# Optimization experiments

Hardware: AMD Instinct MI355X
Metric: run time of the kernel (lower is better)

Reference implementation:

```python
import jax, jax.numpy as jnp
import numpy as np

N = 100000      # nodes
E = 3200000     # edges (avg degree 32)
F_IN = 128      # input features
HID = 16        # hidden channels (hardcoded in Net)
C = 8           # num_classes


def setup_inputs() -> dict:
    key = jax.random.key(0)
    ks = jax.random.split(key, 6)
    x = jax.random.normal(ks[0], (N, F_IN), dtype=jnp.float32)
    edge_index = jax.random.randint(ks[1], (2, E), 0, N, dtype=jnp.int32)
    W1 = jax.random.normal(ks[2], (F_IN, HID), dtype=jnp.float32) / np.sqrt(F_IN)
    b1 = jnp.zeros((HID,), dtype=jnp.float32)
    W2 = jax.random.normal(ks[3], (HID, C), dtype=jnp.float32) / np.sqrt(HID)
    b2 = jnp.zeros((C,), dtype=jnp.float32)
    return {"x": x, "edge_index": edge_index, "W1": W1, "b1": b1, "W2": W2, "b2": b2}


def _gcn_conv(h, W, b, src, dst, norm):
    # GCNConv: x' = D^{-1/2} (A + I) D^{-1/2} (x W) + b
    h = h @ W                                  # [N, out] transform first (small out dim)
    msg = h[src] * norm[:, None]               # gather + edge normalization  [E+N, out]
    agg = jax.ops.segment_sum(msg, dst, num_segments=N)  # scatter-add to targets
    return agg + b


def reference(x, edge_index, W1, b1, W2, b2):
    row, col = edge_index[0], edge_index[1]
    loop = jnp.arange(N, dtype=row.dtype)
    src = jnp.concatenate([row, loop])         # add self-loops
    dst = jnp.concatenate([col, loop])
    # symmetric normalization: deg over aggregation targets (incl. self-loops)
    deg = jax.ops.segment_sum(jnp.ones_like(dst, dtype=jnp.float32), dst, num_segments=N)
    dinv = jnp.where(deg > 0, jax.lax.rsqrt(deg), 0.0)
    norm = dinv[src] * dinv[dst]               # [E+N]

    h = jax.nn.relu(_gcn_conv(x, W1, b1, src, dst, norm))
    # F.dropout with training=False is the identity (inference reference)
    out = _gcn_conv(h, W2, b2, src, dst, norm)
    return jax.nn.log_softmax(out, axis=1)
```

## Files before the change

kernel.cpp:

```cpp
#include <hip/hip_runtime.h>

#define NN 100000
#define EE 3200000
#define FIN 128
#define HID 16
#define NC 8

#define CHUNK 12500
#define NBLK 256
#define BW 256
#define NBUK ((NN + BW - 1) / BW)
#define EPT 13
#define BSTG 10240
#define BEPT 10

__device__ __forceinline__ unsigned bf16pair(float a, float b) {
    unsigned ua = __float_as_uint(a), ub = __float_as_uint(b);
    ua = ua + 0x7fffu + ((ua >> 16) & 1u);
    ub = ub + 0x7fffu + ((ub >> 16) & 1u);
    return (ua >> 16) | (ub & 0xffff0000u);
}

__global__ __launch_bounds__(1024) void k_hist(const int* __restrict__ col,
                                               unsigned* __restrict__ hist_g) {
    __shared__ unsigned h[NBUK];
    int t = threadIdx.x;
    for (int i = t; i < NBUK; i += 1024) h[i] = 0u;
    __syncthreads();
    int base = blockIdx.x * CHUNK;
    for (int i = t; i < CHUNK; i += 1024) {
        int d = col[base + i];
        atomicAdd(&h[d >> 8], 1u);
    }
    __syncthreads();
    for (int b = t; b < NBUK; b += 1024)
        hist_g[(size_t)b * NBLK + blockIdx.x] = h[b];
}

__global__ __launch_bounds__(256) void k_scan_blocks(const unsigned* __restrict__ hist_g,
                                                     unsigned* __restrict__ blockbase,
                                                     unsigned* __restrict__ totals) {
    __shared__ unsigned sc[NBLK];
    int b = blockIdx.x, t = threadIdx.x;
    unsigned v = hist_g[(size_t)b * NBLK + t];
    sc[t] = v;
    __syncthreads();
    for (int off = 1; off < NBLK; off <<= 1) {
        unsigned x = (t >= off) ? sc[t - off] : 0u;
        __syncthreads();
        sc[t] += x;
        __syncthreads();
    }
    blockbase[(size_t)b * NBLK + t] = sc[t] - v;
    if (t == NBLK - 1) totals[b] = sc[t];
}

__global__ __launch_bounds__(512) void k_scan_buckets(const unsigned* __restrict__ totals,
                                                      unsigned* __restrict__ bucket_base) {
    __shared__ unsigned sc[512];
    int t = threadIdx.x;
    unsigned v = (t < NBUK) ? totals[t] : 0u;
    sc[t] = v;
    __syncthreads();
    for (int off = 1; off < 512; off <<= 1) {
        unsigned x = (t >= off) ? sc[t - off] : 0u;
        __syncthreads();
        sc[t] += x;
        __syncthreads();
    }
    if (t < NBUK) bucket_base[t] = sc[t] - v;
    if (t == NBUK - 1) bucket_base[NBUK] = sc[t];
}

__global__ __launch_bounds__(1024) void k_binscatter(const int* __restrict__ row,
                                                     const int* __restrict__ col,
                                                     const unsigned* __restrict__ blockbase,
                                                     const unsigned* __restrict__ bucket_base,
                                                     unsigned* __restrict__ bins_pk) {
    __shared__ unsigned s_cnt[NBUK];
    __shared__ unsigned s_start[NBUK];
    __shared__ unsigned s_off[NBUK];
    __shared__ unsigned s_bb[NBUK];
    __shared__ unsigned stg[CHUNK];
    __shared__ unsigned short bktid[CHUNK];
    int t = threadIdx.x;
    for (int i = t; i < NBUK; i += 1024) {
        s_cnt[i] = 0u;
        s_bb[i] = bucket_base[i] + blockbase[(size_t)i * NBLK + blockIdx.x];
    }
    __syncthreads();
    int base = blockIdx.x * CHUNK;
    unsigned val[EPT];
    unsigned short bk[EPT];
    #pragma unroll
    for (int k = 0; k < EPT; ++k) {
        int i = t + k * 1024;
        if (i < CHUNK) {
            int s = row[base + i];
            int d = col[base + i];
            unsigned b = (unsigned)d >> 8;
            val[k] = (unsigned)s | ((unsigned)(d & 255) << 17);
            bk[k] = (unsigned short)b;
            atomicAdd(&s_cnt[b], 1u);
        }
    }
    __syncthreads();
    for (int off = 1; off < NBUK; off <<= 1) {
        unsigned v = 0u;
        if (t < NBUK && t >= off) v = s_cnt[t - off];
        __syncthreads();
        if (t < NBUK) s_cnt[t] += v;
        __syncthreads();
    }
    if (t < NBUK) {
        unsigned st = (t == 0) ? 0u : s_cnt[t - 1];
        s_start[t] = st;
        s_off[t] = st;
    }
    __syncthreads();
    #pragma unroll
    for (int k = 0; k < EPT; ++k) {
        int i = t + k * 1024;
        if (i < CHUNK) {
            unsigned b = bk[k];
            unsigned r = atomicAdd(&s_off[b], 1u);
            stg[r] = val[k];
            bktid[r] = (unsigned short)b;
        }
    }
    __syncthreads();
    for (int i = t; i < CHUNK; i += 1024) {
        unsigned b = bktid[i];
        bins_pk[s_bb[b] + ((unsigned)i - s_start[b])] = stg[i];
    }
}

__global__ __launch_bounds__(1024) void k_build(const unsigned* __restrict__ bins_pk,
                                                const unsigned* __restrict__ bucket_base,
                                                unsigned* __restrict__ row_ptr,
                                                float* __restrict__ dinv,
                                                unsigned* __restrict__ srcsort) {
    __shared__ unsigned cnt[BW];
    __shared__ unsigned startn[BW];
    __shared__ unsigned offn[BW];
    __shared__ unsigned stg[BSTG];
    int t = threadIdx.x, b = blockIdx.x;
    if (t < BW) cnt[t] = 0u;
    __syncthreads();
    unsigned start = bucket_base[b], end = bucket_base[b + 1];
    unsigned m = end - start;
    unsigned val[BEPT];
    unsigned char dl[BEPT];
    #pragma unroll
    for (int k = 0; k < BEPT; ++k) {
        unsigned i = t + k * 1024u;
        if (i < m) {
            unsigned w = bins_pk[start + i];
            val[k] = w & 0x1FFFFu;
            dl[k] = (unsigned char)(w >> 17);
            atomicAdd(&cnt[dl[k]], 1u);
        }
    }
    __syncthreads();
    for (int off = 1; off < BW; off <<= 1) {
        unsigned v = 0u;
        if (t < BW && t >= off) v = cnt[t - off];
        __syncthreads();
        if (t < BW) cnt[t] += v;
        __syncthreads();
    }
    if (t < BW) {
        unsigned st = (t == 0) ? 0u : cnt[t - 1];
        startn[t] = st;
        offn[t] = st;
        int node = b * BW + t;
        if (node < NN) {
            row_ptr[node] = start + st;
            dinv[node] = rsqrtf(1.0f + (float)(cnt[t] - st));
        }
    }
    if (b == 0 && t == 0) row_ptr[NN] = EE;
    __syncthreads();
    #pragma unroll
    for (int k = 0; k < BEPT; ++k) {
        unsigned i = t + k * 1024u;
        if (i < m) {
            unsigned r = atomicAdd(&offn[dl[k]], 1u);
            stg[r] = val[k];
        }
    }
    __syncthreads();
    for (unsigned i = t; i < m; i += 1024u)
        srcsort[start + i] = stg[i];
}

__global__ __launch_bounds__(256) void k_gemm1(const float* __restrict__ x,
                                               const float* __restrict__ W1,
                                               const float* __restrict__ dinv,
                                               unsigned* __restrict__ hs1b) {
    __shared__ float w1s[FIN * HID];
    __shared__ float xs[64 * 132];
    int t = threadIdx.x;
    int r0 = blockIdx.x * 64;
    for (int i = t; i < FIN * HID; i += 256) w1s[i] = W1[i];
    int maxr = NN - r0; if (maxr > 64) maxr = 64;
    const float4* x4 = reinterpret_cast<const float4*>(x + (size_t)r0 * FIN);
    #pragma unroll
    for (int i = 0; i < 8; ++i) {
        int fi = t + i * 256;
        int f = fi * 4;
        int r = f >> 7, k = f & 127;
        if (r < maxr) {
            float4 v = x4[fi];
            *reinterpret_cast<float4*>(&xs[r * 132 + k]) = v;
        }
    }
    __syncthreads();
    int r = t >> 2;
    int cg = (t & 3) * 4;
    if (r < maxr) {
        float4 acc = {0.f, 0.f, 0.f, 0.f};
        const float* xr = &xs[r * 132];
        #pragma unroll 4
        for (int k = 0; k < FIN; ++k) {
            float xv = xr[k];
            const float4 w = *reinterpret_cast<const float4*>(&w1s[k * HID + cg]);
            acc.x += xv * w.x; acc.y += xv * w.y; acc.z += xv * w.z; acc.w += xv * w.w;
        }
        int rr = r0 + r;
        float di = dinv[rr];
        uint2 pk;
        pk.x = bf16pair(acc.x * di, acc.y * di);
        pk.y = bf16pair(acc.z * di, acc.w * di);
        *reinterpret_cast<uint2*>(&hs1b[(rr << 3) + (cg >> 1)]) = pk;
    }
}

__global__ __launch_bounds__(256) void k_l1(const unsigned* __restrict__ row_ptr,
                                            const unsigned* __restrict__ srcsort,
                                            const unsigned* __restrict__ hs1b,
                                            const float* __restrict__ dinv,
                                            const float* __restrict__ W2,
                                            const float* __restrict__ b1,
                                            unsigned* __restrict__ hs2b) {
    __shared__ float htile[32 * 17];
    __shared__ float w2s[HID * NC];
    int t = threadIdx.x;
    if (t < HID * NC) w2s[t] = W2[t];
    int g = t >> 3;
    int c2 = t & 7;
    int n = blockIdx.x * 32 + g;
    unsigned e0 = row_ptr[n], e1 = row_ptr[n + 1];
    float a0 = 0.f, a1 = 0.f;
    unsigned e = e0;
    for (; e + 3 < e1; e += 4) {
        int s0 = srcsort[e];
        int s1 = srcsort[e + 1];
        int s2 = srcsort[e + 2];
        int s3 = srcsort[e + 3];
        unsigned v0 = hs1b[(s0 << 3) + c2];
        unsigned v1 = hs1b[(s1 << 3) + c2];
        unsigned v2 = hs1b[(s2 << 3) + c2];
        unsigned v3 = hs1b[(s3 << 3) + c2];
        a0 += __uint_as_float(v0 << 16) + __uint_as_float(v1 << 16)
            + __uint_as_float(v2 << 16) + __uint_as_float(v3 << 16);
        a1 += __uint_as_float(v0 & 0xffff0000u) + __uint_as_float(v1 & 0xffff0000u)
            + __uint_as_float(v2 & 0xffff0000u) + __uint_as_float(v3 & 0xffff0000u);
    }
    for (; e < e1; ++e) {
        unsigned v = hs1b[((int)srcsort[e] << 3) + c2];
        a0 += __uint_as_float(v << 16);
        a1 += __uint_as_float(v & 0xffff0000u);
    }
    {
        unsigned v = hs1b[(n << 3) + c2];
        a0 += __uint_as_float(v << 16);
        a1 += __uint_as_float(v & 0xffff0000u);
    }
    float di = dinv[n];
    int c = c2 * 2;
    htile[g * 17 + c]     = fmaxf(a0 * di + b1[c], 0.f);
    htile[g * 17 + c + 1] = fmaxf(a1 * di + b1[c + 1], 0.f);
    __syncthreads();
    if (t < 128) {
        int n2 = t >> 2, j2 = t & 3;
        const float* hr = &htile[n2 * 17];
        float oa = 0.f, ob = 0.f;
        #pragma unroll
        for (int k = 0; k < HID; ++k) {
            float hv = hr[k];
            oa += hv * w2s[k * NC + 2 * j2];
            ob += hv * w2s[k * NC + 2 * j2 + 1];
        }
        int node2 = blockIdx.x * 32 + n2;
        float d2 = dinv[node2];
        hs2b[(node2 << 2) + j2] = bf16pair(oa * d2, ob * d2);
    }
}

__global__ __launch_bounds__(256) void k_l2(const unsigned* __restrict__ row_ptr,
                                            const unsigned* __restrict__ srcsort,
                                            const unsigned* __restrict__ hs2b,
                                            const float* __restrict__ dinv,
                                            const float* __restrict__ b2,
                                            float* __restrict__ out) {
    int t = threadIdx.x;
    int g = t >> 2;
    int c2 = t & 3;
    int n = blockIdx.x * 64 + g;
    if (n >= NN) return;
    unsigned e0 = row_ptr[n], e1 = row_ptr[n + 1];
    float a0 = 0.f, a1 = 0.f;
    unsigned e = e0;
    for (; e + 3 < e1; e += 4) {
        int s0 = srcsort[e];
        int s1 = srcsort[e + 1];
        int s2 = srcsort[e + 2];
        int s3 = srcsort[e + 3];
        unsigned v0 = hs2b[(s0 << 2) + c2];
        unsigned v1 = hs2b[(s1 << 2) + c2];
        unsigned v2 = hs2b[(s2 << 2) + c2];
        unsigned v3 = hs2b[(s3 << 2) + c2];
        a0 += __uint_as_float(v0 << 16) + __uint_as_float(v1 << 16)
            + __uint_as_float(v2 << 16) + __uint_as_float(v3 << 16);
        a1 += __uint_as_float(v0 & 0xffff0000u) + __uint_as_float(v1 & 0xffff0000u)
            + __uint_as_float(v2 & 0xffff0000u) + __uint_as_float(v3 & 0xffff0000u);
    }
    for (; e < e1; ++e) {
        unsigned v = hs2b[((int)srcsort[e] << 2) + c2];
        a0 += __uint_as_float(v << 16);
        a1 += __uint_as_float(v & 0xffff0000u);
    }
    {
        unsigned v = hs2b[(n << 2) + c2];
        a0 += __uint_as_float(v << 16);
        a1 += __uint_as_float(v & 0xffff0000u);
    }
    float di = dinv[n];
    int c = c2 * 2;
    float v0 = a0 * di + b2[c];
    float v1 = a1 * di + b2[c + 1];
    float m = fmaxf(v0, v1);
    m = fmaxf(m, __shfl_xor(m, 1, 4));
    m = fmaxf(m, __shfl_xor(m, 2, 4));
    float s = expf(v0 - m) + expf(v1 - m);
    s += __shfl_xor(s, 1, 4);
    s += __shfl_xor(s, 2, 4);
    float ls = logf(s);
    float2 o = {v0 - m - ls, v1 - m - ls};
    *reinterpret_cast<float2*>(&out[(n << 3) + c]) = o;
}

extern "C" void kernel_launch(void* const* d_in, const int* in_sizes, int n_in,
                              void* d_out, int out_size, void* d_ws, size_t ws_size,
                              hipStream_t stream) {
    const float* x   = (const float*)d_in[0];
    const int*   ei  = (const int*)d_in[1];
    const float* W1  = (const float*)d_in[2];
    const float* b1  = (const float*)d_in[3];
    const float* W2  = (const float*)d_in[4];
    const float* b2  = (const float*)d_in[5];
    float* out = (float*)d_out;

    const int* row = ei;
    const int* col = ei + EE;

    float*    ws          = (float*)d_ws;
    float*    dinv        = ws;
    unsigned* hs1b        = (unsigned*)(dinv + NN);
    unsigned* hs2b        = hs1b + (size_t)NN * 8;
    unsigned* row_ptr     = hs2b + (size_t)NN * 4;
    unsigned* hist_g      = row_ptr + NN + 1;
    unsigned* blockbase   = hist_g + (size_t)NBUK * NBLK;
    unsigned* totals      = blockbase + (size_t)NBUK * NBLK;
    unsigned* bucket_base = totals + NBUK;
    unsigned* bins_pk     = bucket_base + NBUK + 1;
    unsigned* srcsort     = bins_pk + EE;

    k_hist        <<<NBLK, 1024, 0, stream>>>(col, hist_g);
    k_scan_blocks <<<NBUK, NBLK, 0, stream>>>(hist_g, blockbase, totals);
    k_scan_buckets<<<1, 512, 0, stream>>>(totals, bucket_base);
    k_binscatter  <<<NBLK, 1024, 0, stream>>>(row, col, blockbase, bucket_base, bins_pk);
    k_build       <<<NBUK, 1024, 0, stream>>>(bins_pk, bucket_base, row_ptr, dinv, srcsort);
    k_gemm1       <<<(NN + 63) / 64, 256, 0, stream>>>(x, W1, dinv, hs1b);
    k_l1          <<<NN / 32, 256, 0, stream>>>(row_ptr, srcsort, hs1b, dinv, W2, b1, hs2b);
    k_l2          <<<(NN + 63) / 64, 256, 0, stream>>>(row_ptr, srcsort, hs2b, dinv, b2, out);
}
```

Baseline: 114.9 us.

## Replace histogram+scan bucketing with fixed-capacity buckets and atomic cursors

Drops the global histogram kernel and the two prefix-scan kernels. Each binscatter block now reserves its slice of a bucket by doing an atomicAdd on a per-bucket global cursor, and writes into fixed-capacity bucket regions of CAP entries. The CSR offsets become (start,end) pairs per node, because bucket regions are no longer contiguous. This removes two extra launches and a full pass over col. The cost is a bucket-overflow risk if any bucket gets more than 9216 edges (the mean is about 8192), plus padded, non-deterministic edge ordering within buckets.

```diff
diff --git a/kernel.cpp b/kernel.cpp
--- a/kernel.cpp
+++ b/kernel.cpp
@@ -11,8 +11,8 @@
 #define BW 256
 #define NBUK ((NN + BW - 1) / BW)
 #define EPT 13
-#define BSTG 10240
-#define BEPT 10
+#define CAP 9216
+#define BEPT 9
 
 __device__ __forceinline__ unsigned bf16pair(float a, float b) {
     unsigned ua = __float_as_uint(a), ub = __float_as_uint(b);
@@ -21,73 +21,23 @@
     return (ua >> 16) | (ub & 0xffff0000u);
 }
 
-__global__ __launch_bounds__(1024) void k_hist(const int* __restrict__ col,
-                                               unsigned* __restrict__ hist_g) {
-    __shared__ unsigned h[NBUK];
-    int t = threadIdx.x;
-    for (int i = t; i < NBUK; i += 1024) h[i] = 0u;
-    __syncthreads();
-    int base = blockIdx.x * CHUNK;
-    for (int i = t; i < CHUNK; i += 1024) {
-        int d = col[base + i];
-        atomicAdd(&h[d >> 8], 1u);
-    }
-    __syncthreads();
-    for (int b = t; b < NBUK; b += 1024)
-        hist_g[(size_t)b * NBLK + blockIdx.x] = h[b];
-}
-
-__global__ __launch_bounds__(256) void k_scan_blocks(const unsigned* __restrict__ hist_g,
-                                                     unsigned* __restrict__ blockbase,
-                                                     unsigned* __restrict__ totals) {
-    __shared__ unsigned sc[NBLK];
-    int b = blockIdx.x, t = threadIdx.x;
-    unsigned v = hist_g[(size_t)b * NBLK + t];
-    sc[t] = v;
-    __syncthreads();
-    for (int off = 1; off < NBLK; off <<= 1) {
-        unsigned x = (t >= off) ? sc[t - off] : 0u;
-        __syncthreads();
-        sc[t] += x;
-        __syncthreads();
-    }
-    blockbase[(size_t)b * NBLK + t] = sc[t] - v;
-    if (t == NBLK - 1) totals[b] = sc[t];
-}
-
-__global__ __launch_bounds__(512) void k_scan_buckets(const unsigned* __restrict__ totals,
-                                                      unsigned* __restrict__ bucket_base) {
-    __shared__ unsigned sc[512];
-    int t = threadIdx.x;
-    unsigned v = (t < NBUK) ? totals[t] : 0u;
-    sc[t] = v;
-    __syncthreads();
-    for (int off = 1; off < 512; off <<= 1) {
-        unsigned x = (t >= off) ? sc[t - off] : 0u;
-        __syncthreads();
-        sc[t] += x;
-        __syncthreads();
-    }
-    if (t < NBUK) bucket_base[t] = sc[t] - v;
-    if (t == NBUK - 1) bucket_base[NBUK] = sc[t];
+__global__ __launch_bounds__(512) void k_zero_cursor(unsigned* __restrict__ cursor) {
+    int t = threadIdx.x;
+    if (t < NBUK) cursor[t] = 0u;
 }
 
 __global__ __launch_bounds__(1024) void k_binscatter(const int* __restrict__ row,
                                                      const int* __restrict__ col,
-                                                     const unsigned* __restrict__ blockbase,
-                                                     const unsigned* __restrict__ bucket_base,
+                                                     unsigned* __restrict__ cursor,
                                                      unsigned* __restrict__ bins_pk) {
     __shared__ unsigned s_cnt[NBUK];
     __shared__ unsigned s_start[NBUK];
     __shared__ unsigned s_off[NBUK];
-    __shared__ unsigned s_bb[NBUK];
+    __shared__ unsigned s_gb[NBUK];
     __shared__ unsigned stg[CHUNK];
     __shared__ unsigned short bktid[CHUNK];
     int t = threadIdx.x;
-    for (int i = t; i < NBUK; i += 1024) {
-        s_cnt[i] = 0u;
-        s_bb[i] = bucket_base[i] + blockbase[(size_t)i * NBLK + blockIdx.x];
-    }
+    for (int i = t; i < NBUK; i += 1024) s_cnt[i] = 0u;
     __syncthreads();
     int base = blockIdx.x * CHUNK;
     unsigned val[EPT];
@@ -105,6 +55,9 @@
         }
     }
     __syncthreads();
+    for (int i = t; i < NBUK; i += 1024)
+        s_gb[i] = atomicAdd(&cursor[i], s_cnt[i]);
+    __syncthreads();
     for (int off = 1; off < NBUK; off <<= 1) {
         unsigned v = 0u;
         if (t < NBUK && t >= off) v = s_cnt[t - off];
@@ -131,31 +84,30 @@
     __syncthreads();
     for (int i = t; i < CHUNK; i += 1024) {
         unsigned b = bktid[i];
-        bins_pk[s_bb[b] + ((unsigned)i - s_start[b])] = stg[i];
+        bins_pk[(size_t)b * CAP + s_gb[b] + ((unsigned)i - s_start[b])] = stg[i];
     }
 }
 
 __global__ __launch_bounds__(1024) void k_build(const unsigned* __restrict__ bins_pk,
-                                                const unsigned* __restrict__ bucket_base,
-                                                unsigned* __restrict__ row_ptr,
+                                                const unsigned* __restrict__ cursor,
+                                                uint2* __restrict__ row_se,
                                                 float* __restrict__ dinv,
                                                 unsigned* __restrict__ srcsort) {
     __shared__ unsigned cnt[BW];
-    __shared__ unsigned startn[BW];
     __shared__ unsigned offn[BW];
-    __shared__ unsigned stg[BSTG];
+    __shared__ unsigned stg[CAP];
     int t = threadIdx.x, b = blockIdx.x;
     if (t < BW) cnt[t] = 0u;
     __syncthreads();
-    unsigned start = bucket_base[b], end = bucket_base[b + 1];
-    unsigned m = end - start;
+    unsigned m = cursor[b];
+    unsigned base = (unsigned)b * CAP;
     unsigned val[BEPT];
     unsigned char dl[BEPT];
     #pragma unroll
     for (int k = 0; k < BEPT; ++k) {
         unsigned i = t + k * 1024u;
         if (i < m) {
-            unsigned w = bins_pk[start + i];
+            unsigned w = bins_pk[base + i];
             val[k] = w & 0x1FFFFu;
             dl[k] = (unsigned char)(w >> 17);
             atomicAdd(&cnt[dl[k]], 1u);
@@ -171,15 +123,13 @@
     }
     if (t < BW) {
         unsigned st = (t == 0) ? 0u : cnt[t - 1];
-        startn[t] = st;
         offn[t] = st;
         int node = b * BW + t;
         if (node < NN) {
-            row_ptr[node] = start + st;
+            row_se[node] = uint2{base + st, base + cnt[t]};
             dinv[node] = rsqrtf(1.0f + (float)(cnt[t] - st));
         }
     }
-    if (b == 0 && t == 0) row_ptr[NN] = EE;
     __syncthreads();
     #pragma unroll
     for (int k = 0; k < BEPT; ++k) {
@@ -191,7 +141,7 @@
     }
     __syncthreads();
     for (unsigned i = t; i < m; i += 1024u)
-        srcsort[start + i] = stg[i];
+        srcsort[base + i] = stg[i];
 }
 
 __global__ __launch_bounds__(256) void k_gemm1(const float* __restrict__ x,
@@ -236,7 +186,7 @@
     }
 }
 
-__global__ __launch_bounds__(256) void k_l1(const unsigned* __restrict__ row_ptr,
+__global__ __launch_bounds__(256) void k_l1(const uint2* __restrict__ row_se,
                                             const unsigned* __restrict__ srcsort,
                                             const unsigned* __restrict__ hs1b,
                                             const float* __restrict__ dinv,
@@ -250,9 +200,9 @@
     int g = t >> 3;
     int c2 = t & 7;
     int n = blockIdx.x * 32 + g;
-    unsigned e0 = row_ptr[n], e1 = row_ptr[n + 1];
+    uint2 se = row_se[n];
+    unsigned e = se.x, e1 = se.y;
     float a0 = 0.f, a1 = 0.f;
-    unsigned e = e0;
     for (; e + 3 < e1; e += 4) {
         int s0 = srcsort[e];
         int s1 = srcsort[e + 1];
@@ -298,7 +248,7 @@
     }
 }
 
-__global__ __launch_bounds__(256) void k_l2(const unsigned* __restrict__ row_ptr,
+__global__ __launch_bounds__(256) void k_l2(const uint2* __restrict__ row_se,
                                             const unsigned* __restrict__ srcsort,
                                             const unsigned* __restrict__ hs2b,
                                             const float* __restrict__ dinv,
@@ -309,9 +259,9 @@
     int c2 = t & 3;
     int n = blockIdx.x * 64 + g;
     if (n >= NN) return;
-    unsigned e0 = row_ptr[n], e1 = row_ptr[n + 1];
+    uint2 se = row_se[n];
+    unsigned e = se.x, e1 = se.y;
     float a0 = 0.f, a1 = 0.f;
-    unsigned e = e0;
     for (; e + 3 < e1; e += 4) {
         int s0 = srcsort[e];
         int s1 = srcsort[e + 1];
@@ -365,24 +315,19 @@
     const int* row = ei;
     const int* col = ei + EE;
 
-    float*    ws          = (float*)d_ws;
-    float*    dinv        = ws;
-    unsigned* hs1b        = (unsigned*)(dinv + NN);
-    unsigned* hs2b        = hs1b + (size_t)NN * 8;
-    unsigned* row_ptr     = hs2b + (size_t)NN * 4;
-    unsigned* hist_g      = row_ptr + NN + 1;
-    unsigned* blockbase   = hist_g + (size_t)NBUK * NBLK;
-    unsigned* totals      = blockbase + (size_t)NBUK * NBLK;
-    unsigned* bucket_base = totals + NBUK;
-    unsigned* bins_pk     = bucket_base + NBUK + 1;
-    unsigned* srcsort     = bins_pk + EE;
-
-    k_hist        <<<NBLK, 1024, 0, stream>>>(col, hist_g);
-    k_scan_blocks <<<NBUK, NBLK, 0, stream>>>(hist_g, blockbase, totals);
-    k_scan_buckets<<<1, 512, 0, stream>>>(totals, bucket_base);
-    k_binscatter  <<<NBLK, 1024, 0, stream>>>(row, col, blockbase, bucket_base, bins_pk);
-    k_build       <<<NBUK, 1024, 0, stream>>>(bins_pk, bucket_base, row_ptr, dinv, srcsort);
+    float*    ws      = (float*)d_ws;
+    float*    dinv    = ws;
+    unsigned* hs1b    = (unsigned*)(dinv + NN);
+    unsigned* hs2b    = hs1b + (size_t)NN * 8;
+    uint2*    row_se  = (uint2*)(hs2b + (size_t)NN * 4);
+    unsigned* cursor  = (unsigned*)(row_se + NN);
+    unsigned* bins_pk = cursor + NBUK;
+    unsigned* srcsort = bins_pk + (size_t)NBUK * CAP;
+
+    k_zero_cursor <<<1, 512, 0, stream>>>(cursor);
+    k_binscatter  <<<NBLK, 1024, 0, stream>>>(row, col, cursor, bins_pk);
+    k_build       <<<NBUK, 1024, 0, stream>>>(bins_pk, cursor, row_se, dinv, srcsort);
     k_gemm1       <<<(NN + 63) / 64, 256, 0, stream>>>(x, W1, dinv, hs1b);
-    k_l1          <<<NN / 32, 256, 0, stream>>>(row_ptr, srcsort, hs1b, dinv, W2, b1, hs2b);
-    k_l2          <<<(NN + 63) / 64, 256, 0, stream>>>(row_ptr, srcsort, hs2b, dinv, b2, out);
-}
+    k_l1          <<<NN / 32, 256, 0, stream>>>(row_se, srcsort, hs1b, dinv, W2, b1, hs2b);
+    k_l2          <<<(NN + 63) / 64, 256, 0, stream>>>(row_se, srcsort, hs2b, dinv, b2, out);
+}
```

Result: faster. 112.1 us (-2.4%).
